# Kernel optimization log

Hardware: AMD Instinct MI355X
Metric: run time of the kernel (lower is better)

## Reference

```python
import jax, jax.numpy as jnp
import numpy as np

D_MODEL = 1024
LN_EPS = 1e-5


def setup_inputs() -> dict:
    key = jax.random.key(0)
    k_u, k_b, k_c = jax.random.split(key, 3)
    B, L, D = 8, 4096, D_MODEL
    u = jax.random.normal(k_u, (B, L, D), dtype=jnp.float32)
    # parameters (torch init analogues)
    log_a = jnp.log(jnp.linspace(0.9, 0.99, D, dtype=jnp.float32))
    bound = 1.0 / np.sqrt(D)
    W_b = jax.random.uniform(k_b, (D, D), minval=-bound, maxval=bound, dtype=jnp.float32)
    W_c = jax.random.uniform(k_c, (D, D), minval=-bound, maxval=bound, dtype=jnp.float32)
    gamma = jnp.ones((D,), dtype=jnp.float32)
    beta = jnp.zeros((D,), dtype=jnp.float32)
    return {"u": u, "log_a": log_a, "W_b": W_b, "W_c": W_c, "gamma": gamma, "beta": beta}


def reference(u, log_a, W_b, W_c, gamma, beta):
    # u: [B, L, D]; diagonal LTI SSM: state_t = a * state_{t-1} + (u_t @ W_b^T)
    B, L, D = u.shape
    a = jnp.exp(log_a)  # [D]
    u_b = jnp.einsum('bld,ed->ble', u, W_b)  # batched b-projection over all timesteps

    def step(state, ub_t):
        state = a * state + ub_t
        return state, state

    init = jnp.zeros((B, D), dtype=u.dtype)
    _, states = jax.lax.scan(step, init, jnp.swapaxes(u_b, 0, 1))  # [L, B, D]
    states = jnp.swapaxes(states, 0, 1)  # [B, L, D]

    y = jnp.einsum('bld,ed->ble', states, W_c)  # c-projection batched over time

    # LayerNorm over last dim
    mean = jnp.mean(y, axis=-1, keepdims=True)
    var = jnp.mean(jnp.square(y - mean), axis=-1, keepdims=True)
    return gamma * (y - mean) * jax.lax.rsqrt(var + LN_EPS) + beta
```

## Files before the change

kernel.cpp:

```cpp
#include <hip/hip_runtime.h>
#include <hip/hip_bf16.h>
#include <math.h>

#define B_SZ 8
#define L_SZ 4096
#define D_SZ 1024
#define CHT  64
#define NCH  (L_SZ / CHT)

typedef __bf16 bf16_t;
typedef bf16_t bf16x8 __attribute__((ext_vector_type(8)));
typedef bf16_t bf16x4 __attribute__((ext_vector_type(4)));
typedef float  f32x4  __attribute__((ext_vector_type(4)));

#define BM 256
#define BN 256
#define BK 32
#define NT 32
#define BUFB 32768
#define EP_P 68

__device__ __forceinline__ void gld16(const void* g, void* l) {
  __builtin_amdgcn_global_load_lds(
      (const __attribute__((address_space(1))) void*)g,
      (__attribute__((address_space(3))) void*)l, 16, 0, 0);
}

#define MFMA16(a, b, c) __builtin_amdgcn_mfma_f32_16x16x32_bf16(a, b, c, 0, 0, 0)

template<int MODE>
__global__ __launch_bounds__(512, 1)
void gemm256(const bf16_t* __restrict__ A, const bf16_t* __restrict__ Wt,
             bf16_t* __restrict__ Cg, const float* __restrict__ pw,
             float* __restrict__ cf) {
  __shared__ __align__(16) char smem[3 * BUFB];
  const int tid  = threadIdx.x;
  const int lane = tid & 63;
  const int wave = tid >> 6;
  const int wm = wave >> 2, wn = wave & 3;
  const int fr = lane & 15, g = lane >> 4;

  const int flat = (blockIdx.x & 7) * 64 + (blockIdx.x >> 3);
  const int bx = flat & 3, by = flat >> 2;
  const int brow = by * BM, bcol = bx * BN;

  const int ll  = lane >> 3;
  const int sl  = (lane & 7) ^ ll;
  const int srw = ll * 2 + (sl >> 2);
  const int sch = sl & 3;
  const bf16_t* aSrc = A  + (size_t)(brow + wave * 32 + srw) * 1024 + sch * 8;
  const bf16_t* bSrc = Wt + (size_t)(bcol + wave * 32 + srw) * 1024 + sch * 8;

  const int h = fr >> 1;
  const int slotv = (((fr & 1) << 2) | g) ^ h;
  const int aoff = wm * 8192 + h * 128 + slotv * 16;
  const int boff = 16384 + wn * 4096 + h * 128 + slotv * 16;

#define STG(DB, T) { \
    char* d_ = (DB) + wave * 2048; \
    const size_t ko_ = (size_t)(T) * BK; \
    gld16(aSrc + ko_, d_); \
    gld16(aSrc + (size_t)16 * 1024 + ko_, d_ + 1024); \
    gld16(bSrc + ko_, d_ + 16384); \
    gld16(bSrc + (size_t)16 * 1024 + ko_, d_ + 17408); \
  }

  f32x4 acc[8][4] = {};
  bf16x8 af[8], bfv[4];

  STG(smem, 0);
  STG(smem + BUFB, 1);
  asm volatile("s_waitcnt vmcnt(4)" ::: "memory");
  __builtin_amdgcn_s_barrier();
  asm volatile("" ::: "memory");

  int bu = 0, bs = 2;
  for (int t = 0; t < NT; ++t) {
    const char* sb = smem + bu * BUFB;
#pragma unroll
    for (int m = 0; m < 8; ++m)
      af[m] = *(const bf16x8*)(sb + aoff + m * 1024);
#pragma unroll
    for (int n = 0; n < 4; ++n)
      bfv[n] = *(const bf16x8*)(sb + boff + n * 1024);
    if (t + 2 < NT) STG(smem + bs * BUFB, t + 2);
    __builtin_amdgcn_s_setprio(1);
#pragma unroll
    for (int m = 0; m < 8; ++m)
#pragma unroll
      for (int n = 0; n < 4; ++n)
        acc[m][n] = MFMA16(af[m], bfv[n], acc[m][n]);
    __builtin_amdgcn_s_setprio(0);
    if (t + 2 < NT) asm volatile("s_waitcnt vmcnt(4)" ::: "memory");
    else            asm volatile("s_waitcnt vmcnt(0)" ::: "memory");
    __builtin_amdgcn_s_barrier();
    asm volatile("" ::: "memory");
    bu = (bu == 2) ? 0 : bu + 1;
    bs = (bs == 2) ? 0 : bs + 1;
  }
#undef STG

  __syncthreads();
  float* strip = (float*)smem;
  const int bb  = by >> 4;
  const int cg0 = (by & 15) * 4;
#pragma unroll 1
  for (int q = 0; q < 4; ++q) {
    if (wn == q) {
#pragma unroll
      for (int mi = 0; mi < 8; ++mi)
#pragma unroll
        for (int ni = 0; ni < 4; ++ni)
#pragma unroll
          for (int r = 0; r < 4; ++r)
            strip[(wm * 128 + mi * 16 + g * 4 + r) * EP_P + ni * 16 + fr] = acc[mi][ni][r];
    }
    __syncthreads();
    if constexpr (MODE == 0) {
      if (tid < 256) {
        const int col = tid & 63;
        const int ch  = tid >> 6;
        const int d   = bcol + q * 64 + col;
        const float a = pw[d];
        float s = 0.f;
#pragma unroll 1
        for (int grp = 0; grp < 4; ++grp) {
          float v[16];
#pragma unroll
          for (int u = 0; u < 16; ++u) v[u] = strip[(ch * 64 + grp * 16 + u) * EP_P + col];
#pragma unroll
          for (int u = 0; u < 16; ++u) { s = a * s + v[u]; v[u] = s; }
#pragma unroll
          for (int u = 0; u < 16; ++u) strip[(ch * 64 + grp * 16 + u) * EP_P + col] = v[u];
        }
        cf[((size_t)(bb * NCH + cg0 + ch)) * D_SZ + d] = s;
      }
      __syncthreads();
    }
#pragma unroll
    for (int j = 0; j < 4; ++j) {
      const int u = j * 512 + tid;
      const int row = u >> 3;
      const int cu = (u & 7) * 8;
      f32x4 lo = *(const f32x4*)&strip[row * EP_P + cu];
      f32x4 hi = *(const f32x4*)&strip[row * EP_P + cu + 4];
      bf16x8 h2;
#pragma unroll
      for (int jj = 0; jj < 4; ++jj) { h2[jj] = (bf16_t)lo[jj]; h2[4 + jj] = (bf16_t)hi[jj]; }
      *(bf16x8*)&Cg[(size_t)(brow + row) * 1024 + bcol + q * 64 + cu] = h2;
    }
    __syncthreads();
  }
}

__global__ __launch_bounds__(256)
void conv_bf16_k(const float* __restrict__ src, bf16_t* __restrict__ dst, int n) {
  int i = (blockIdx.x * 256 + threadIdx.x) * 4;
  const int stride = gridDim.x * 256 * 4;
  for (; i < n; i += stride) {
    f32x4 v = *(const f32x4*)(src + i);
    bf16x4 h;
#pragma unroll
    for (int j = 0; j < 4; ++j) h[j] = (bf16_t)v[j];
    *(bf16x4*)(dst + i) = h;
  }
}

__global__ __launch_bounds__(256)
void pow_k(const float* __restrict__ log_a, float* __restrict__ pw) {
  const int t = blockIdx.x;
  const int d = threadIdx.x * 4;
#pragma unroll
  for (int j = 0; j < 4; ++j)
    pw[t * D_SZ + d + j] = expf(log_a[d + j] * (float)(t + 1));
}

__global__ __launch_bounds__(256)
void scan_carry_k(const float* __restrict__ log_a, float* __restrict__ cf) {
  const int d = blockIdx.x * 256 + threadIdx.x;
  const int b = blockIdx.y;
  const float aT = expf(log_a[d] * (float)CHT);
  float s = 0.f;
  for (int c = 0; c < NCH; ++c) {
    const size_t idx = ((size_t)(b * NCH + c)) * D_SZ + d;
    s = aT * s + cf[idx];
    cf[idx] = s;
  }
}

__global__ __launch_bounds__(128)
void scan_apply_k(const bf16_t* __restrict__ xb16, const float* __restrict__ pw,
                  const float* __restrict__ cf, bf16_t* __restrict__ xs16) {
  const int d8 = threadIdx.x * 8;
  const int l = blockIdx.x;
  const int b = blockIdx.y;
  const int c = l >> 6;
  const int t = l & (CHT - 1);
  const size_t idx = ((size_t)(b * L_SZ + l)) * D_SZ + d8;
  bf16x8 hv = *(const bf16x8*)(xb16 + idx);
  float s[8];
#pragma unroll
  for (int j = 0; j < 8; ++j) s[j] = (float)hv[j];
  if (c > 0) {
    f32x4 p0  = *(const f32x4*)(pw + t * D_SZ + d8);
    f32x4 p1  = *(const f32x4*)(pw + t * D_SZ + d8 + 4);
    const float* cb = cf + ((size_t)(b * NCH + (c - 1))) * D_SZ + d8;
    f32x4 v0 = *(const f32x4*)cb;
    f32x4 v1 = *(const f32x4*)(cb + 4);
#pragma unroll
    for (int j = 0; j < 4; ++j) { s[j] += p0[j] * v0[j]; s[4 + j] += p1[j] * v1[j]; }
  }
  bf16x8 h;
#pragma unroll
  for (int j = 0; j < 8; ++j) h[j] = (bf16_t)s[j];
  *(bf16x8*)(xs16 + idx) = h;
}

__global__ __launch_bounds__(256)
void ln_k(const bf16_t* __restrict__ y, const float* __restrict__ gamma,
          const float* __restrict__ beta, float* __restrict__ out) {
  const size_t row = blockIdx.x;
  const int tid = threadIdx.x;
  bf16x4 h = *(const bf16x4*)(y + row * D_SZ + tid * 4);
  float v[4];
#pragma unroll
  for (int j = 0; j < 4; ++j) v[j] = (float)h[j];
  float s  = v[0] + v[1] + v[2] + v[3];
  float sq = v[0] * v[0] + v[1] * v[1] + v[2] * v[2] + v[3] * v[3];
#pragma unroll
  for (int off = 32; off; off >>= 1) {
    s  += __shfl_down(s, off);
    sq += __shfl_down(sq, off);
  }
  __shared__ float red[8];
  const int wid = tid >> 6;
  if ((tid & 63) == 0) { red[wid] = s; red[4 + wid] = sq; }
  __syncthreads();
  s  = red[0] + red[1] + red[2] + red[3];
  sq = red[4] + red[5] + red[6] + red[7];
  const float mean = s * (1.f / D_SZ);
  const float var  = sq * (1.f / D_SZ) - mean * mean;
  const float inv  = rsqrtf(var + 1e-5f);
  f32x4 gm = *(const f32x4*)(gamma + tid * 4);
  f32x4 bt = *(const f32x4*)(beta  + tid * 4);
  f32x4 o;
#pragma unroll
  for (int j = 0; j < 4; ++j) o[j] = (v[j] - mean) * inv * gm[j] + bt[j];
  *(f32x4*)(out + row * D_SZ + tid * 4) = o;
}

extern "C" void kernel_launch(void* const* d_in, const int* in_sizes, int n_in,
                              void* d_out, int out_size, void* d_ws, size_t ws_size,
                              hipStream_t stream) {
  const float* u     = (const float*)d_in[0];
  const float* log_a = (const float*)d_in[1];
  const float* W_b   = (const float*)d_in[2];
  const float* W_c   = (const float*)d_in[3];
  const float* gamma = (const float*)d_in[4];
  const float* beta  = (const float*)d_in[5];
  float* out = (float*)d_out;

  const size_t NBLD = (size_t)B_SZ * L_SZ * D_SZ;
  bf16_t* u16  = (bf16_t*)d_ws;
  bf16_t* xb16 = u16 + NBLD;
  bf16_t* wb16 = xb16 + NBLD;
  bf16_t* wc16 = wb16 + (size_t)D_SZ * D_SZ;
  float*  cf   = (float*)(wc16 + (size_t)D_SZ * D_SZ);
  float*  pw   = cf + (size_t)B_SZ * NCH * D_SZ;
  bf16_t* xs16 = u16;
  bf16_t* y16  = xb16;

  const int nblk = (B_SZ * L_SZ / BM) * (D_SZ / BN);

  conv_bf16_k<<<2048, 256, 0, stream>>>(u, u16, (int)NBLD);
  conv_bf16_k<<<512, 256, 0, stream>>>(W_b, wb16, D_SZ * D_SZ);
  conv_bf16_k<<<512, 256, 0, stream>>>(W_c, wc16, D_SZ * D_SZ);
  pow_k<<<CHT, 256, 0, stream>>>(log_a, pw);

  gemm256<0><<<nblk, 512, 0, stream>>>(u16, wb16, xb16, pw, cf);
  scan_carry_k<<<dim3(D_SZ / 256, B_SZ), 256, 0, stream>>>(log_a, cf);
  scan_apply_k<<<dim3(L_SZ, B_SZ), 128, 0, stream>>>(xb16, pw, cf, xs16);
  gemm256<1><<<nblk, 512, 0, stream>>>(xs16, wc16, y16, nullptr, nullptr);
  ln_k<<<B_SZ * L_SZ, 256, 0, stream>>>(y16, gamma, beta, out);
}
```

Baseline: 261.3 us.

## Fuse fp32-to-bf16 conversion of input into first GEMM's A-tile loads

Removes the separate conversion kernel for the large activation tensor u. The first GEMM now loads fp32 rows into registers, converts them to bf16 and writes them swizzled into LDS one stage ahead, while B still uses direct global-to-LDS loads. This saves a full read and write of a bf16 copy of u, at the cost of doubled A-side global traffic per tile, extra registers, and VALU conversion work inside the pipelined loop.

```diff
diff --git a/kernel.cpp b/kernel.cpp
--- a/kernel.cpp
+++ b/kernel.cpp
@@ -28,11 +28,169 @@
 
 #define MFMA16(a, b, c) __builtin_amdgcn_mfma_f32_16x16x32_bf16(a, b, c, 0, 0, 0)
 
-template<int MODE>
 __global__ __launch_bounds__(512, 1)
-void gemm256(const bf16_t* __restrict__ A, const bf16_t* __restrict__ Wt,
+void gemm1_k(const float* __restrict__ U, const bf16_t* __restrict__ Wt,
              bf16_t* __restrict__ Cg, const float* __restrict__ pw,
              float* __restrict__ cf) {
+  __shared__ __align__(16) char smem[3 * BUFB];
+  const int tid  = threadIdx.x;
+  const int lane = tid & 63;
+  const int wave = tid >> 6;
+  const int wm = wave >> 2, wn = wave & 3;
+  const int fr = lane & 15, g = lane >> 4;
+
+  const int flat = (blockIdx.x & 7) * 64 + (blockIdx.x >> 3);
+  const int bx = flat & 3, by = flat >> 2;
+  const int brow = by * BM, bcol = bx * BN;
+
+  const float* uA = U + (size_t)(brow + wave * 32 + (lane >> 2)) * 1024 + (lane & 3) * 8;
+  const int r0 = lane >> 2;
+  const int awoff = wave * 2048 + (r0 >> 1) * 128 +
+                    (((((r0 & 1) << 2) | (lane & 3)) ^ (r0 >> 1)) << 4);
+
+  const int ll  = lane >> 3;
+  const int sl  = (lane & 7) ^ ll;
+  const int srw = ll * 2 + (sl >> 2);
+  const int sch = sl & 3;
+  const bf16_t* bSrc = Wt + (size_t)(bcol + wave * 32 + srw) * 1024 + sch * 8;
+  const int bldsoff = 16384 + wave * 2048;
+
+  const int h = fr >> 1;
+  const int slotv = (((fr & 1) << 2) | g) ^ h;
+  const int aoff = wm * 8192 + h * 128 + slotv * 16;
+  const int boff = 16384 + wn * 4096 + h * 128 + slotv * 16;
+
+  f32x4 acc[8][4] = {};
+  f32x4 ra0, ra1, ra2, ra3, rb0, rb1, rb2, rb3;
+
+  {
+    const float* g0 = uA;
+    ra0 = *(const f32x4*)(g0);              ra1 = *(const f32x4*)(g0 + 4);
+    ra2 = *(const f32x4*)(g0 + 16 * 1024);  ra3 = *(const f32x4*)(g0 + 16 * 1024 + 4);
+    gld16(bSrc, smem + bldsoff);
+    gld16(bSrc + (size_t)16 * 1024, smem + bldsoff + 1024);
+    const float* g1 = uA + BK;
+    rb0 = *(const f32x4*)(g1);              rb1 = *(const f32x4*)(g1 + 4);
+    rb2 = *(const f32x4*)(g1 + 16 * 1024);  rb3 = *(const f32x4*)(g1 + 16 * 1024 + 4);
+    gld16(bSrc + BK, smem + BUFB + bldsoff);
+    gld16(bSrc + (size_t)16 * 1024 + BK, smem + BUFB + bldsoff + 1024);
+  }
+  asm volatile("s_waitcnt vmcnt(0)" ::: "memory");
+  {
+    bf16x8 h0, h1;
+#pragma unroll
+    for (int j = 0; j < 4; ++j) {
+      h0[j] = (bf16_t)ra0[j]; h0[4 + j] = (bf16_t)ra1[j];
+      h1[j] = (bf16_t)ra2[j]; h1[4 + j] = (bf16_t)ra3[j];
+    }
+    *(bf16x8*)(smem + awoff) = h0;
+    *(bf16x8*)(smem + awoff + 1024) = h1;
+  }
+  asm volatile("s_waitcnt lgkmcnt(0)" ::: "memory");
+  __builtin_amdgcn_s_barrier();
+  asm volatile("" ::: "memory");
+
+#define BODY(T, N0, N1, N2, N3, F0, F1, F2, F3) do { \
+    const char* sb_ = smem + ((T) % 3) * BUFB; \
+    bf16x8 af_[8], bv_[4]; \
+    _Pragma("unroll") \
+    for (int m = 0; m < 8; ++m) af_[m] = *(const bf16x8*)(sb_ + aoff + m * 1024); \
+    _Pragma("unroll") \
+    for (int n = 0; n < 4; ++n) bv_[n] = *(const bf16x8*)(sb_ + boff + n * 1024); \
+    if ((T) + 2 < NT) { \
+      char* db_ = smem + (((T) + 2) % 3) * BUFB + bldsoff; \
+      const size_t ko_ = (size_t)((T) + 2) * BK; \
+      gld16(bSrc + ko_, db_); \
+      gld16(bSrc + (size_t)16 * 1024 + ko_, db_ + 1024); \
+      const float* gp_ = uA + ko_; \
+      F0 = *(const f32x4*)(gp_);              F1 = *(const f32x4*)(gp_ + 4); \
+      F2 = *(const f32x4*)(gp_ + 16 * 1024); F3 = *(const f32x4*)(gp_ + 16 * 1024 + 4); \
+    } \
+    __builtin_amdgcn_s_setprio(1); \
+    _Pragma("unroll") \
+    for (int m = 0; m < 8; ++m) \
+      _Pragma("unroll") \
+      for (int n = 0; n < 4; ++n) \
+        acc[m][n] = MFMA16(af_[m], bv_[n], acc[m][n]); \
+    __builtin_amdgcn_s_setprio(0); \
+    if ((T) + 2 < NT) { asm volatile("s_waitcnt vmcnt(6)" ::: "memory"); } \
+    else              { asm volatile("s_waitcnt vmcnt(0)" ::: "memory"); } \
+    if ((T) + 1 < NT) { \
+      char* wb_ = smem + (((T) + 1) % 3) * BUFB; \
+      bf16x8 h0_, h1_; \
+      _Pragma("unroll") \
+      for (int j = 0; j < 4; ++j) { \
+        h0_[j] = (bf16_t)N0[j]; h0_[4 + j] = (bf16_t)N1[j]; \
+        h1_[j] = (bf16_t)N2[j]; h1_[4 + j] = (bf16_t)N3[j]; \
+      } \
+      *(bf16x8*)(wb_ + awoff) = h0_; \
+      *(bf16x8*)(wb_ + awoff + 1024) = h1_; \
+    } \
+    asm volatile("s_waitcnt lgkmcnt(0)" ::: "memory"); \
+    __builtin_amdgcn_s_barrier(); \
+    asm volatile("" ::: "memory"); \
+  } while (0)
+
+  for (int t = 0; t < NT; t += 2) {
+    BODY(t,     rb0, rb1, rb2, rb3, ra0, ra1, ra2, ra3);
+    BODY(t + 1, ra0, ra1, ra2, ra3, rb0, rb1, rb2, rb3);
+  }
+#undef BODY
+
+  __syncthreads();
+  float* strip = (float*)smem;
+  const int bb  = by >> 4;
+  const int cg0 = (by & 15) * 4;
+#pragma unroll 1
+  for (int q = 0; q < 4; ++q) {
+    if (wn == q) {
+#pragma unroll
+      for (int mi = 0; mi < 8; ++mi)
+#pragma unroll
+        for (int ni = 0; ni < 4; ++ni)
+#pragma unroll
+          for (int r = 0; r < 4; ++r)
+            strip[(wm * 128 + mi * 16 + g * 4 + r) * EP_P + ni * 16 + fr] = acc[mi][ni][r];
+    }
+    __syncthreads();
+    if (tid < 256) {
+      const int col = tid & 63;
+      const int ch  = tid >> 6;
+      const int d   = bcol + q * 64 + col;
+      const float a = pw[d];
+      float s = 0.f;
+#pragma unroll 1
+      for (int grp = 0; grp < 4; ++grp) {
+        float v[16];
+#pragma unroll
+        for (int u = 0; u < 16; ++u) v[u] = strip[(ch * 64 + grp * 16 + u) * EP_P + col];
+#pragma unroll
+        for (int u = 0; u < 16; ++u) { s = a * s + v[u]; v[u] = s; }
+#pragma unroll
+        for (int u = 0; u < 16; ++u) strip[(ch * 64 + grp * 16 + u) * EP_P + col] = v[u];
+      }
+      cf[((size_t)(bb * NCH + cg0 + ch)) * D_SZ + d] = s;
+    }
+    __syncthreads();
+#pragma unroll
+    for (int j = 0; j < 4; ++j) {
+      const int u = j * 512 + tid;
+      const int row = u >> 3;
+      const int cu = (u & 7) * 8;
+      f32x4 lo = *(const f32x4*)&strip[row * EP_P + cu];
+      f32x4 hi = *(const f32x4*)&strip[row * EP_P + cu + 4];
+      bf16x8 h2;
+#pragma unroll
+      for (int jj = 0; jj < 4; ++jj) { h2[jj] = (bf16_t)lo[jj]; h2[4 + jj] = (bf16_t)hi[jj]; }
+      *(bf16x8*)&Cg[(size_t)(brow + row) * 1024 + bcol + q * 64 + cu] = h2;
+    }
+    __syncthreads();
+  }
+}
+
+__global__ __launch_bounds__(512, 1)
+void gemm2_k(const bf16_t* __restrict__ A, const bf16_t* __restrict__ Wt,
+             bf16_t* __restrict__ Cg) {
   __shared__ __align__(16) char smem[3 * BUFB];
   const int tid  = threadIdx.x;
   const int lane = tid & 63;
@@ -102,8 +260,6 @@
 
   __syncthreads();
   float* strip = (float*)smem;
-  const int bb  = by >> 4;
-  const int cg0 = (by & 15) * 4;
 #pragma unroll 1
   for (int q = 0; q < 4; ++q) {
     if (wn == q) {
@@ -116,27 +272,6 @@
             strip[(wm * 128 + mi * 16 + g * 4 + r) * EP_P + ni * 16 + fr] = acc[mi][ni][r];
     }
     __syncthreads();
-    if constexpr (MODE == 0) {
-      if (tid < 256) {
-        const int col = tid & 63;
-        const int ch  = tid >> 6;
-        const int d   = bcol + q * 64 + col;
-        const float a = pw[d];
-        float s = 0.f;
-#pragma unroll 1
-        for (int grp = 0; grp < 4; ++grp) {
-          float v[16];
-#pragma unroll
-          for (int u = 0; u < 16; ++u) v[u] = strip[(ch * 64 + grp * 16 + u) * EP_P + col];
-#pragma unroll
-          for (int u = 0; u < 16; ++u) { s = a * s + v[u]; v[u] = s; }
-#pragma unroll
-          for (int u = 0; u < 16; ++u) strip[(ch * 64 + grp * 16 + u) * EP_P + col] = v[u];
-        }
-        cf[((size_t)(bb * NCH + cg0 + ch)) * D_SZ + d] = s;
-      }
-      __syncthreads();
-    }
 #pragma unroll
     for (int j = 0; j < 4; ++j) {
       const int u = j * 512 + tid;
@@ -261,25 +396,23 @@
   float* out = (float*)d_out;
 
   const size_t NBLD = (size_t)B_SZ * L_SZ * D_SZ;
-  bf16_t* u16  = (bf16_t*)d_ws;
-  bf16_t* xb16 = u16 + NBLD;
+  bf16_t* xs16 = (bf16_t*)d_ws;
+  bf16_t* xb16 = xs16 + NBLD;
   bf16_t* wb16 = xb16 + NBLD;
   bf16_t* wc16 = wb16 + (size_t)D_SZ * D_SZ;
   float*  cf   = (float*)(wc16 + (size_t)D_SZ * D_SZ);
   float*  pw   = cf + (size_t)B_SZ * NCH * D_SZ;
-  bf16_t* xs16 = u16;
   bf16_t* y16  = xb16;
 
   const int nblk = (B_SZ * L_SZ / BM) * (D_SZ / BN);
 
-  conv_bf16_k<<<2048, 256, 0, stream>>>(u, u16, (int)NBLD);
   conv_bf16_k<<<512, 256, 0, stream>>>(W_b, wb16, D_SZ * D_SZ);
   conv_bf16_k<<<512, 256, 0, stream>>>(W_c, wc16, D_SZ * D_SZ);
   pow_k<<<CHT, 256, 0, stream>>>(log_a, pw);
 
-  gemm256<0><<<nblk, 512, 0, stream>>>(u16, wb16, xb16, pw, cf);
+  gemm1_k<<<nblk, 512, 0, stream>>>(u, wb16, xb16, pw, cf);
   scan_carry_k<<<dim3(D_SZ / 256, B_SZ), 256, 0, stream>>>(log_a, cf);
   scan_apply_k<<<dim3(L_SZ, B_SZ), 128, 0, stream>>>(xb16, pw, cf, xs16);
-  gemm256<1><<<nblk, 512, 0, stream>>>(xs16, wc16, y16, nullptr, nullptr);
+  gemm2_k<<<nblk, 512, 0, stream>>>(xs16, wc16, y16);
   ln_k<<<B_SZ * L_SZ, 256, 0, stream>>>(y16, gamma, beta, out);
 }
```

Result: slower. 275.1 us (+5.3%).
